# Performance work log

Hardware: AMD Instinct MI355X
Metric: run time of the kernel (lower is better)

Reference implementation:

```python
import jax, jax.numpy as jnp
import numpy as np

DEPTH, DIM, HEADS, MLP, P, IMG, C = 6, 512, 8, 2048, 16, 224, 3
NPATCH = (IMG // P) ** 2  # 196
EPS = 1e-5


def setup_inputs() -> dict:
    key = jax.random.key(0)
    ks = jax.random.split(key, 16)
    s = 0.02
    return {
        "img": jax.random.normal(ks[0], (64, C, IMG, IMG), jnp.float32),
        "patch_w": jax.random.normal(ks[1], (DIM, C * P * P), jnp.float32) * s,
        "patch_b": jax.random.normal(ks[2], (DIM,), jnp.float32) * s,
        "cls_token": jax.random.normal(ks[3], (1, 1, DIM), jnp.float32),
        "pos_emb": jax.random.normal(ks[4], (1, NPATCH + 1, DIM), jnp.float32),
        "in_proj_w": jax.random.normal(ks[5], (DEPTH, 3 * DIM, DIM), jnp.float32) * s,
        "in_proj_b": jax.random.normal(ks[6], (DEPTH, 3 * DIM), jnp.float32) * s,
        "out_proj_w": jax.random.normal(ks[7], (DEPTH, DIM, DIM), jnp.float32) * s,
        "out_proj_b": jax.random.normal(ks[8], (DEPTH, DIM), jnp.float32) * s,
        "ln1_w": jnp.ones((DEPTH, DIM), jnp.float32),
        "ln1_b": jnp.zeros((DEPTH, DIM), jnp.float32),
        "fc1_w": jax.random.normal(ks[9], (DEPTH, MLP, DIM), jnp.float32) * s,
        "fc1_b": jax.random.normal(ks[10], (DEPTH, MLP), jnp.float32) * s,
        "fc2_w": jax.random.normal(ks[11], (DEPTH, DIM, MLP), jnp.float32) * s,
        "fc2_b": jax.random.normal(ks[12], (DEPTH, DIM), jnp.float32) * s,
        "ln2_w": jnp.ones((DEPTH, DIM), jnp.float32),
        "ln2_b": jnp.zeros((DEPTH, DIM), jnp.float32),
    }


def _ln(x, w, b):
    m = jnp.mean(x, -1, keepdims=True)
    v = jnp.mean(jnp.square(x - m), -1, keepdims=True)
    return (x - m) * jax.lax.rsqrt(v + EPS) * w + b


def _patchify(img):
    # b c (h p1) (w p2) -> b (h w) (p1 p2 c), lucidrains ViT ordering
    B = img.shape[0]
    g = IMG // P
    x = img.reshape(B, C, g, P, g, P)
    x = x.transpose(0, 2, 4, 3, 5, 1)  # B, h, w, p1, p2, c
    return x.reshape(B, g * g, P * P * C)


def _vit(img, patch_w, patch_b, cls_token, pos_emb, in_proj_w, in_proj_b,
         out_proj_w, out_proj_b, ln1_w, ln1_b, fc1_w, fc1_b, fc2_w, fc2_b,
         ln2_w, ln2_b):
    B = img.shape[0]
    hd = DIM // HEADS
    x = _patchify(img) @ patch_w.T + patch_b          # [B, 196, 512]
    cls = jnp.broadcast_to(cls_token, (B, 1, DIM))
    x = jnp.concatenate([cls, x], axis=1) + pos_emb   # [B, 197, 512]
    N = x.shape[1]
    for i in range(DEPTH):
        res = x
        qkv = x @ in_proj_w[i].T + in_proj_b[i]       # [B, N, 3*512]
        q, k, v = jnp.split(qkv, 3, axis=-1)
        q = q.reshape(B, N, HEADS, hd).transpose(0, 2, 1, 3)
        k = k.reshape(B, N, HEADS, hd).transpose(0, 2, 1, 3)
        v = v.reshape(B, N, HEADS, hd).transpose(0, 2, 1, 3)
        scores = jnp.einsum('bhnd,bhmd->bhnm', q, k) / jnp.sqrt(jnp.float32(hd))
        probs = jax.nn.softmax(scores, axis=-1)
        ctx = jnp.einsum('bhnm,bhmd->bhnd', probs, v)
        ctx = ctx.transpose(0, 2, 1, 3).reshape(B, N, DIM)
        x = ctx @ out_proj_w[i].T + out_proj_b[i] + res
        x = _ln(x, ln1_w[i], ln1_b[i])
        res = x
        h = jax.nn.gelu(x @ fc1_w[i].T + fc1_b[i], approximate=False)
        x = h @ fc2_w[i].T + fc2_b[i] + res
        x = _ln(x, ln2_w[i], ln2_b[i])
    return x[:, 0]  # ToCLS_Slice: forward returns CLS token [B, 512]


def reference(img, patch_w, patch_b, cls_token, pos_emb, in_proj_w, in_proj_b,
              out_proj_w, out_proj_b, ln1_w, ln1_b, fc1_w, fc1_b, fc2_w, fc2_b,
              ln2_w, ln2_b):
    return _vit(img, patch_w, patch_b, cls_token, pos_emb, in_proj_w, in_proj_b,
                out_proj_w, out_proj_b, ln1_w, ln1_b, fc1_w, fc1_b, fc2_w, fc2_b,
                ln2_w, ln2_b)
```

## Files before the change

kernel.cpp:

```cpp
#include <hip/hip_runtime.h>
#include <hip/hip_bf16.h>

typedef __hip_bfloat16 hb;
typedef __bf16 bf16x8 __attribute__((ext_vector_type(8)));
typedef float f32x4 __attribute__((ext_vector_type(4)));

#define N_DEPTH 6
#define N_DIM   512
#define N_HEADS 8
#define N_MLP   2048
#define N_TOK   197
#define N_PATCH 196
#define N_BATCH 64
#define ROWS    (N_BATCH * N_TOK)
#define ROWS_PAD 12672
#define PROWS   (N_BATCH * N_PATCH)

#define OFF_WPATCH 0u
#define OFF_WQKV   786432u
#define OFF_WOUT   10223616u
#define OFF_WFC1   13369344u
#define OFF_WFC2   25952256u
#define OFF_XBF    38535168u
#define OFF_CTX    51511296u
#define OFF_BIG    64487424u
#define OFF_XF     116391936u
#define OFF_H1     142344192u

__device__ __forceinline__ void gl2lds(const hb* g, hb* l) {
    __builtin_amdgcn_global_load_lds((const __attribute__((address_space(1))) unsigned int*)g,
                                     (__attribute__((address_space(3))) unsigned int*)l, 16, 0, 0);
}


__global__ void cvt_bf16_kernel(const float* __restrict__ in, hb* __restrict__ out, int n) {
    int t = blockIdx.x * 256 + threadIdx.x;
    if (t < n) out[t] = __float2bfloat16(in[t]);
}

__global__ void patchify_kernel(const float* __restrict__ img, hb* __restrict__ Xp) {
    int t = blockIdx.x * 256 + threadIdx.x;
    if (t >= PROWS * 768) return;
    int r = t / 768, j = t % 768;
    int b = r / 196, p = r % 196;
    int ph = p / 14, pw = p % 14;
    int p1 = j / 48, jr = j % 48;
    int p2 = jr / 3, c = jr % 3;
    float v = img[(((size_t)b * 3 + c) * 224 + ph * 16 + p1) * 224 + pw * 16 + p2];
    Xp[t] = __float2bfloat16(v);
}

__global__ void cls_init_kernel(const float* __restrict__ cls, const float* __restrict__ pos,
                                float* __restrict__ xf, hb* __restrict__ xb) {
    int t = blockIdx.x * 256 + threadIdx.x;
    int b = t >> 9, c = t & 511;
    float v = cls[c] + pos[c];
    size_t off = ((size_t)b * N_TOK) * N_DIM + c;
    xf[off] = v;
    xb[off] = __float2bfloat16(v);
}

__global__ void zero_pads_kernel(float* __restrict__ xf, hb* __restrict__ xb, hb* __restrict__ ctx) {
    int t = blockIdx.x * 256 + threadIdx.x;
    size_t off = (size_t)ROWS * N_DIM + t;
    xf[off] = 0.f;
    xb[off] = __float2bfloat16(0.f);
    ctx[off] = __float2bfloat16(0.f);
}

__global__ void extract_cls_kernel(const float* __restrict__ xf, float* __restrict__ out) {
    int t = blockIdx.x * 256 + threadIdx.x;
    int b = t >> 9, c = t & 511;
    out[t] = xf[((size_t)b * N_TOK) * N_DIM + c];
}


__global__ void __launch_bounds__(256) ln_kernel(const float* __restrict__ in,
                                                 const float* __restrict__ w, const float* __restrict__ b,
                                                 float* __restrict__ outf, hb* __restrict__ outb, int rows) {
    int row = blockIdx.x * 4 + (threadIdx.x >> 6);
    int lane = threadIdx.x & 63;
    if (row >= rows) return;
    const float* p = in + (size_t)row * N_DIM;
    float4 v0 = *(const float4*)(p + lane * 8);
    float4 v1 = *(const float4*)(p + lane * 8 + 4);
    float xs[8] = {v0.x, v0.y, v0.z, v0.w, v1.x, v1.y, v1.z, v1.w};
    float s = 0.f, q = 0.f;
#pragma unroll
    for (int j = 0; j < 8; ++j) { s += xs[j]; q += xs[j] * xs[j]; }
#pragma unroll
    for (int o = 32; o > 0; o >>= 1) { s += __shfl_xor(s, o); q += __shfl_xor(q, o); }
    float mean = s * (1.f / 512.f);
    float var = q * (1.f / 512.f) - mean * mean;
    float r = rsqrtf(var + 1e-5f);
    float4 w0 = *(const float4*)(w + lane * 8);
    float4 w1 = *(const float4*)(w + lane * 8 + 4);
    float4 b0 = *(const float4*)(b + lane * 8);
    float4 b1 = *(const float4*)(b + lane * 8 + 4);
    float ws8[8] = {w0.x, w0.y, w0.z, w0.w, w1.x, w1.y, w1.z, w1.w};
    float bs8[8] = {b0.x, b0.y, b0.z, b0.w, b1.x, b1.y, b1.z, b1.w};
    float of[8] __attribute__((aligned(16)));
    hb tb[8] __attribute__((aligned(16)));
#pragma unroll
    for (int j = 0; j < 8; ++j) {
        float y = (xs[j] - mean) * r * ws8[j] + bs8[j];
        of[j] = y;
        tb[j] = __float2bfloat16(y);
    }
    *(float4*)(outf + (size_t)row * N_DIM + lane * 8)     = *(const float4*)&of[0];
    *(float4*)(outf + (size_t)row * N_DIM + lane * 8 + 4) = *(const float4*)&of[4];
    *(float4*)(outb + (size_t)row * N_DIM + lane * 8)     = *(const float4*)&tb[0];
}


template <int MODE>
__global__ void __launch_bounds__(256) gemm_bt(const hb* __restrict__ A, const hb* __restrict__ B,
                                               const float* __restrict__ bias, int K, int N,
                                               hb* __restrict__ outb, float* __restrict__ outf,
                                               const float* __restrict__ res, const float* __restrict__ pos,
                                               hb* __restrict__ vtg) {
    __shared__ hb Sm[8192];
    hb* As = Sm;
    hb* Bs = Sm + 4096;
    const int tid = threadIdx.x;
    const int lane = tid & 63, wid = tid >> 6;
    const int wr = wid >> 1, wc = wid & 1;
    const int quad = lane >> 4, r16 = lane & 15;
    const int m0 = blockIdx.y * 128, n0 = blockIdx.x * 128;

    const int r0 = lane >> 2, c0 = lane & 3;
    const hb* ga0 = A + (size_t)(m0 + wid * 32 + r0) * K + c0 * 8;
    const hb* ga1 = ga0 + (size_t)16 * K;
    const hb* gb0 = B + (size_t)(n0 + wid * 32 + r0) * K + c0 * 8;
    const hb* gb1 = gb0 + (size_t)16 * K;
    hb* la0 = As + (wid * 32) * 32;
    hb* la1 = As + (wid * 32 + 16) * 32;
    hb* lb0 = Bs + (wid * 32) * 32;
    hb* lb1 = Bs + (wid * 32 + 16) * 32;

    f32x4 acc[4][4] = {};

    for (int k0 = 0; k0 < K; k0 += 32) {
        gl2lds(ga0, la0);
        gl2lds(ga1, la1);
        gl2lds(gb0, lb0);
        gl2lds(gb1, lb1);
        ga0 += 32; ga1 += 32; gb0 += 32; gb1 += 32;
        __syncthreads();
        bf16x8 af[4], bfr[4];
#pragma unroll
        for (int t = 0; t < 4; ++t) {
            af[t]  = *(const bf16x8*)&As[(wr * 64 + t * 16 + r16) * 32 + quad * 8];
            bfr[t] = *(const bf16x8*)&Bs[(wc * 64 + t * 16 + r16) * 32 + quad * 8];
        }
#pragma unroll
        for (int mi = 0; mi < 4; ++mi)
#pragma unroll
            for (int nj = 0; nj < 4; ++nj)
                acc[mi][nj] = __builtin_amdgcn_mfma_f32_16x16x32_bf16(af[mi], bfr[nj], acc[mi][nj], 0, 0, 0);
        __syncthreads();
    }

    if constexpr (MODE == 0 || MODE == 1) {
        const bool isv = (MODE == 0) && (n0 >= 1024);
        if (!isv) {
            hb* Cb = Sm + wid * 2048;
#pragma unroll
            for (int p = 0; p < 2; ++p) {
#pragma unroll
                for (int nj2 = 0; nj2 < 2; ++nj2) {
                    int nj = p * 2 + nj2;
                    float bv = bias[n0 + wc * 64 + nj * 16 + r16];
#pragma unroll
                    for (int mi = 0; mi < 4; ++mi)
#pragma unroll
                        for (int e = 0; e < 4; ++e) {
                            float v = acc[mi][nj][e] + bv;
                            if constexpr (MODE == 1)
                                v = 0.5f * v * (1.f + erff(v * 0.70710678118654752f));
                            Cb[(mi * 16 + quad * 4 + e) * 32 + nj2 * 16 + r16] = __float2bfloat16(v);
                        }
                }
#pragma unroll
                for (int it = 0; it < 4; ++it) {
                    int idx = it * 64 + lane;
                    int row = idx >> 2, ch = idx & 3;
                    bf16x8 val = *(const bf16x8*)&Cb[row * 32 + ch * 8];
                    *(bf16x8*)(outb + (size_t)(m0 + wr * 64 + row) * N + n0 + wc * 64 + p * 32 + ch * 8) = val;
                }
            }
        } else {
#pragma unroll
            for (int mi = 0; mi < 4; ++mi) {
#pragma unroll
                for (int e = 0; e < 4; ++e) {
                    int row = m0 + wr * 64 + mi * 16 + quad * 4 + e;
                    int bb = row / 197;
                    int mm = row - bb * 197;
#pragma unroll
                    for (int nj = 0; nj < 4; ++nj) {
                        int col = n0 + wc * 64 + nj * 16 + r16;
                        float v = acc[mi][nj][e] + bias[col];
                        hb hv = __float2bfloat16(v);
                        outb[(size_t)row * N + col] = hv;
                        if (bb < 64) {
                            int d = col - 1024;
                            vtg[((size_t)(bb * 8 + (d >> 6))) * (64 * 224) + (size_t)(d & 63) * 224 + mm] = hv;
                        }
                    }
                }
            }
        }
    } else {
#pragma unroll
        for (int nj = 0; nj < 4; ++nj) {
            int col = n0 + wc * 64 + nj * 16 + r16;
            float bv = bias[col];
#pragma unroll
            for (int mi = 0; mi < 4; ++mi) {
#pragma unroll
                for (int e = 0; e < 4; ++e) {
                    int row = m0 + wr * 64 + mi * 16 + quad * 4 + e;
                    float v = acc[mi][nj][e] + bv;
                    if constexpr (MODE == 2) {
                        v += res[(size_t)row * N + col];
                        outf[(size_t)row * N + col] = v;
                    } else {
                        int pidx = row % 196;
                        int row2 = row + row / 196 + 1;
                        v += pos[(size_t)(pidx + 1) * N_DIM + col];
                        outf[(size_t)row2 * N_DIM + col] = v;
                        outb[(size_t)row2 * N_DIM + col] = __float2bfloat16(v);
                    }
                }
            }
        }
    }
}


__global__ void __launch_bounds__(256, 2) attn_kernel(const hb* __restrict__ qkv,
                                                      const hb* __restrict__ vtg,
                                                      hb* __restrict__ ctx) {
    __shared__ hb Ks[224 * 64];
    __shared__ hb Vt[64 * 224];
    __shared__ hb Pb[4][16 * 40];
    const int bh = blockIdx.x;
    const int b = bh >> 3, h = bh & 7;
    const int tid = threadIdx.x, lane = tid & 63, wid = tid >> 6;
    const int quad = lane >> 4, r16 = lane & 15;
    const hb* base = qkv + (size_t)(b * N_TOK) * 1536 + h * 64;
    const hb* vbase = vtg + (size_t)bh * (64 * 224);

#pragma unroll
    for (int i = 0; i < 7; ++i) {
        int idx = tid + i * 256;
        int m = idx >> 3, c = idx & 7;
        bf16x8 val = {};
        if (m < 197) val = *(const bf16x8*)(base + (size_t)m * 1536 + 512 + c * 8);
        *(bf16x8*)&Ks[m * 64 + c * 8] = val;
    }
#pragma unroll
    for (int i = 0; i < 6; ++i) {
        int idx = tid + i * 256;
        int d = idx / 24, mc = idx % 24;
        *(bf16x8*)&Vt[d * 224 + mc * 8] = *(const bf16x8*)(vbase + d * 224 + mc * 8);
    }
    const hb hzero = __float2bfloat16(0.f);
#pragma unroll
    for (int i = 0; i < 8; ++i) {
        int idx = tid + i * 256;
        int d = idx >> 5, m = 192 + (idx & 31);
        Vt[d * 224 + m] = (m < 197) ? vbase[d * 224 + m] : hzero;
    }

    bf16x8 af[4][2];
#pragma unroll
    for (int mi = 0; mi < 4; ++mi) {
        int q = wid * 64 + mi * 16 + r16;
#pragma unroll
        for (int kc = 0; kc < 2; ++kc)
            af[mi][kc] = *(const bf16x8*)(base + (size_t)q * 1536 + kc * 32 + quad * 8);
    }

    f32x4 o[4][4] = {};
    float mst[4][4], lp[4][4];
#pragma unroll
    for (int mi = 0; mi < 4; ++mi)
#pragma unroll
        for (int e = 0; e < 4; ++e) { mst[mi][e] = -3.0e38f; lp[mi][e] = 0.f; }

    __syncthreads();

    for (int kt = 0; kt < 7; ++kt) {
        bf16x8 bk[2][2], bv[4];
#pragma unroll
        for (int nj = 0; nj < 2; ++nj)
#pragma unroll
            for (int kc = 0; kc < 2; ++kc)
                bk[nj][kc] = *(const bf16x8*)&Ks[(kt * 32 + nj * 16 + r16) * 64 + kc * 32 + quad * 8];
#pragma unroll
        for (int jd = 0; jd < 4; ++jd)
            bv[jd] = *(const bf16x8*)&Vt[(jd * 16 + r16) * 224 + kt * 32 + quad * 8];

        const bool v0 = (kt * 32 + r16) < N_TOK;
        const bool v1 = (kt * 32 + 16 + r16) < N_TOK;

#pragma unroll
        for (int mi = 0; mi < 4; ++mi) {
            f32x4 z = {};
            f32x4 s0v = __builtin_amdgcn_mfma_f32_16x16x32_bf16(af[mi][0], bk[0][0], z, 0, 0, 0);
            s0v = __builtin_amdgcn_mfma_f32_16x16x32_bf16(af[mi][1], bk[0][1], s0v, 0, 0, 0);
            f32x4 s1v = __builtin_amdgcn_mfma_f32_16x16x32_bf16(af[mi][0], bk[1][0], z, 0, 0, 0);
            s1v = __builtin_amdgcn_mfma_f32_16x16x32_bf16(af[mi][1], bk[1][1], s1v, 0, 0, 0);

            float al[4];
#pragma unroll
            for (int e = 0; e < 4; ++e) {
                float s0 = v0 ? s0v[e] * 0.125f : -1e30f;
                float s1 = v1 ? s1v[e] * 0.125f : -1e30f;
                float mx = fmaxf(s0, s1);
#pragma unroll
                for (int off = 1; off < 16; off <<= 1) mx = fmaxf(mx, __shfl_xor(mx, off));
                float mnew = fmaxf(mst[mi][e], mx);
                float alpha = __expf(mst[mi][e] - mnew);
                mst[mi][e] = mnew;
                float p0 = __expf(s0 - mnew);
                float p1 = __expf(s1 - mnew);
                lp[mi][e] = lp[mi][e] * alpha + p0 + p1;
                al[e] = alpha;
                int prow = (quad * 4 + e) * 40;
                Pb[wid][prow + r16]      = __float2bfloat16(p0);
                Pb[wid][prow + 16 + r16] = __float2bfloat16(p1);
            }
#pragma unroll
            for (int jd = 0; jd < 4; ++jd)
#pragma unroll
                for (int e = 0; e < 4; ++e) o[mi][jd][e] *= al[e];
            bf16x8 ap = *(const bf16x8*)&Pb[wid][r16 * 40 + quad * 8];
#pragma unroll
            for (int jd = 0; jd < 4; ++jd)
                o[mi][jd] = __builtin_amdgcn_mfma_f32_16x16x32_bf16(ap, bv[jd], o[mi][jd], 0, 0, 0);
        }
    }

#pragma unroll
    for (int mi = 0; mi < 4; ++mi) {
        float rl[4];
#pragma unroll
        for (int e = 0; e < 4; ++e) {
            float l = lp[mi][e];
#pragma unroll
            for (int off = 1; off < 16; off <<= 1) l += __shfl_xor(l, off);
            rl[e] = 1.f / l;
        }
        int qrow = wid * 64 + mi * 16 + quad * 4;
#pragma unroll
        for (int e = 0; e < 4; ++e) {
            int q = qrow + e;
            if (q < N_TOK) {
                hb* dst = ctx + ((size_t)(b * N_TOK + q)) * N_DIM + h * 64;
#pragma unroll
                for (int jd = 0; jd < 4; ++jd)
                    dst[jd * 16 + r16] = __float2bfloat16(o[mi][jd][e] * rl[e]);
            }
        }
    }
}


extern "C" void kernel_launch(void* const* d_in, const int* in_sizes, int n_in,
                              void* d_out, int out_size, void* d_ws, size_t ws_size,
                              hipStream_t stream) {
    (void)in_sizes; (void)n_in; (void)out_size; (void)ws_size;
    const float* img     = (const float*)d_in[0];
    const float* patch_w = (const float*)d_in[1];
    const float* patch_b = (const float*)d_in[2];
    const float* cls_t   = (const float*)d_in[3];
    const float* pos     = (const float*)d_in[4];
    const float* w_qkv   = (const float*)d_in[5];
    const float* b_qkv   = (const float*)d_in[6];
    const float* w_out   = (const float*)d_in[7];
    const float* b_out   = (const float*)d_in[8];
    const float* ln1w    = (const float*)d_in[9];
    const float* ln1b    = (const float*)d_in[10];
    const float* w_fc1   = (const float*)d_in[11];
    const float* b_fc1   = (const float*)d_in[12];
    const float* w_fc2   = (const float*)d_in[13];
    const float* b_fc2   = (const float*)d_in[14];
    const float* ln2w    = (const float*)d_in[15];
    const float* ln2b    = (const float*)d_in[16];

    char* ws = (char*)d_ws;
    hb* wPatch = (hb*)(ws + OFF_WPATCH);
    hb* wQKV   = (hb*)(ws + OFF_WQKV);
    hb* wOut   = (hb*)(ws + OFF_WOUT);
    hb* wFc1   = (hb*)(ws + OFF_WFC1);
    hb* wFc2   = (hb*)(ws + OFF_WFC2);
    hb* x_bf   = (hb*)(ws + OFF_XBF);
    hb* ctx    = (hb*)(ws + OFF_CTX);
    hb* Xp     = (hb*)(ws + OFF_BIG);
    hb* qkv    = (hb*)(ws + OFF_BIG);
    hb* hmid   = (hb*)(ws + OFF_BIG);
    float* x_f = (float*)(ws + OFF_XF);
    float* h1  = (float*)(ws + OFF_H1);
    hb* vtg    = (hb*)(ws + OFF_H1);

    auto cvt = [&](const float* src, hb* dst, int n) {
        cvt_bf16_kernel<<<dim3((n + 255) / 256), dim3(256), 0, stream>>>(src, dst, n);
    };
    cvt(patch_w, wPatch, 512 * 768);
    cvt(w_qkv, wQKV, N_DEPTH * 1536 * 512);
    cvt(w_out, wOut, N_DEPTH * 512 * 512);
    cvt(w_fc1, wFc1, N_DEPTH * 2048 * 512);
    cvt(w_fc2, wFc2, N_DEPTH * 512 * 2048);

    patchify_kernel<<<dim3((PROWS * 768 + 255) / 256), dim3(256), 0, stream>>>(img, Xp);
    gemm_bt<3><<<dim3(4, 98), dim3(256), 0, stream>>>(Xp, wPatch, patch_b, 768, 512, x_bf, x_f, nullptr, pos, nullptr);
    cls_init_kernel<<<dim3(128), dim3(256), 0, stream>>>(cls_t, pos, x_f, x_bf);
    zero_pads_kernel<<<dim3(128), dim3(256), 0, stream>>>(x_f, x_bf, ctx);

    for (int i = 0; i < N_DEPTH; ++i) {
        gemm_bt<0><<<dim3(12, 99), dim3(256), 0, stream>>>(x_bf, wQKV + (size_t)i * 1536 * 512,
                                                           b_qkv + i * 1536, 512, 1536, qkv, nullptr, nullptr, nullptr, vtg);
        attn_kernel<<<dim3(512), dim3(256), 0, stream>>>(qkv, vtg, ctx);
        gemm_bt<2><<<dim3(4, 99), dim3(256), 0, stream>>>(ctx, wOut + (size_t)i * 512 * 512,
                                                          b_out + i * 512, 512, 512, nullptr, h1, x_f, nullptr, nullptr);
        ln_kernel<<<dim3(3152), dim3(256), 0, stream>>>(h1, ln1w + i * 512, ln1b + i * 512, x_f, x_bf, ROWS);
        gemm_bt<1><<<dim3(16, 99), dim3(256), 0, stream>>>(x_bf, wFc1 + (size_t)i * 2048 * 512,
                                                           b_fc1 + i * 2048, 512, 2048, hmid, nullptr, nullptr, nullptr, nullptr);
        gemm_bt<2><<<dim3(4, 99), dim3(256), 0, stream>>>(hmid, wFc2 + (size_t)i * 512 * 2048,
                                                          b_fc2 + i * 512, 2048, 512, nullptr, h1, x_f, nullptr, nullptr);
        ln_kernel<<<dim3(3152), dim3(256), 0, stream>>>(h1, ln2w + i * 512, ln2b + i * 512, x_f, x_bf, ROWS);
    }

    extract_cls_kernel<<<dim3(128), dim3(256), 0, stream>>>(x_f, (float*)d_out);
}
```

Measured before the change: 1.746 ms.

## Split-K the out-proj and FC2 GEMMs, fuse partial sum into LayerNorm, tanh GELU

```diff
diff --git a/kernel.cpp b/kernel.cpp
--- a/kernel.cpp
+++ b/kernel.cpp
@@ -26,6 +26,8 @@
 #define OFF_BIG    64487424u
 #define OFF_XF     116391936u
 #define OFF_H1     142344192u
+#define OFF_EXTRA  168296448u
+#define WS_NEED_SPLIT (OFF_EXTRA + 25952256u)
 
 __device__ __forceinline__ void gl2lds(const hb* g, hb* l) {
     __builtin_amdgcn_global_load_lds((const __attribute__((address_space(1))) unsigned int*)g,
@@ -75,7 +77,9 @@
 }
 
 
+template <int SUM>
 __global__ void __launch_bounds__(256) ln_kernel(const float* __restrict__ in,
+                                                 const float* __restrict__ in2,
                                                  const float* __restrict__ w, const float* __restrict__ b,
                                                  float* __restrict__ outf, hb* __restrict__ outb, int rows) {
     int row = blockIdx.x * 4 + (threadIdx.x >> 6);
@@ -85,6 +89,13 @@
     float4 v0 = *(const float4*)(p + lane * 8);
     float4 v1 = *(const float4*)(p + lane * 8 + 4);
     float xs[8] = {v0.x, v0.y, v0.z, v0.w, v1.x, v1.y, v1.z, v1.w};
+    if constexpr (SUM) {
+        const float* p2 = in2 + (size_t)row * N_DIM;
+        float4 u0 = *(const float4*)(p2 + lane * 8);
+        float4 u1 = *(const float4*)(p2 + lane * 8 + 4);
+        xs[0] += u0.x; xs[1] += u0.y; xs[2] += u0.z; xs[3] += u0.w;
+        xs[4] += u1.x; xs[5] += u1.y; xs[6] += u1.z; xs[7] += u1.w;
+    }
     float s = 0.f, q = 0.f;
 #pragma unroll
     for (int j = 0; j < 8; ++j) { s += xs[j]; q += xs[j] * xs[j]; }
@@ -115,8 +126,9 @@
 
 template <int MODE>
 __global__ void __launch_bounds__(256) gemm_bt(const hb* __restrict__ A, const hb* __restrict__ B,
-                                               const float* __restrict__ bias, int K, int N,
+                                               const float* __restrict__ bias, int Kstride, int halfK, int N,
                                                hb* __restrict__ outb, float* __restrict__ outf,
+                                               float* __restrict__ outf2,
                                                const float* __restrict__ res, const float* __restrict__ pos,
                                                hb* __restrict__ vtg) {
     __shared__ hb Sm[8192];
@@ -127,12 +139,13 @@
     const int wr = wid >> 1, wc = wid & 1;
     const int quad = lane >> 4, r16 = lane & 15;
     const int m0 = blockIdx.y * 128, n0 = blockIdx.x * 128;
+    const int kb = blockIdx.z * halfK;
 
     const int r0 = lane >> 2, c0 = lane & 3;
-    const hb* ga0 = A + (size_t)(m0 + wid * 32 + r0) * K + c0 * 8;
-    const hb* ga1 = ga0 + (size_t)16 * K;
-    const hb* gb0 = B + (size_t)(n0 + wid * 32 + r0) * K + c0 * 8;
-    const hb* gb1 = gb0 + (size_t)16 * K;
+    const hb* ga0 = A + (size_t)(m0 + wid * 32 + r0) * Kstride + kb + c0 * 8;
+    const hb* ga1 = ga0 + (size_t)16 * Kstride;
+    const hb* gb0 = B + (size_t)(n0 + wid * 32 + r0) * Kstride + kb + c0 * 8;
+    const hb* gb1 = gb0 + (size_t)16 * Kstride;
     hb* la0 = As + (wid * 32) * 32;
     hb* la1 = As + (wid * 32 + 16) * 32;
     hb* lb0 = Bs + (wid * 32) * 32;
@@ -140,7 +153,7 @@
 
     f32x4 acc[4][4] = {};
 
-    for (int k0 = 0; k0 < K; k0 += 32) {
+    for (int k0 = 0; k0 < halfK; k0 += 32) {
         gl2lds(ga0, la0);
         gl2lds(ga1, la1);
         gl2lds(gb0, lb0);
@@ -176,8 +189,11 @@
 #pragma unroll
                         for (int e = 0; e < 4; ++e) {
                             float v = acc[mi][nj][e] + bv;
-                            if constexpr (MODE == 1)
-                                v = 0.5f * v * (1.f + erff(v * 0.70710678118654752f));
+                            if constexpr (MODE == 1) {
+                                float y = 0.79788456f * (v + 0.044715f * v * v * v);
+                                float t = 1.f - 2.f / (__expf(2.f * y) + 1.f);
+                                v = 0.5f * v * (1.f + t);
+                            }
                             Cb[(mi * 16 + quad * 4 + e) * 32 + nj2 * 16 + r16] = __float2bfloat16(v);
                         }
                 }
@@ -211,29 +227,50 @@
                 }
             }
         }
+    } else if constexpr (MODE == 2) {
+        if (blockIdx.z == 0) {
+#pragma unroll
+            for (int nj = 0; nj < 4; ++nj) {
+                int col = n0 + wc * 64 + nj * 16 + r16;
+                float bv = bias[col];
+#pragma unroll
+                for (int mi = 0; mi < 4; ++mi)
+#pragma unroll
+                    for (int e = 0; e < 4; ++e) {
+                        int row = m0 + wr * 64 + mi * 16 + quad * 4 + e;
+                        outf[(size_t)row * N + col] = acc[mi][nj][e] + bv + res[(size_t)row * N + col];
+                    }
+            }
+        } else {
+#pragma unroll
+            for (int nj = 0; nj < 4; ++nj) {
+                int col = n0 + wc * 64 + nj * 16 + r16;
+#pragma unroll
+                for (int mi = 0; mi < 4; ++mi)
+#pragma unroll
+                    for (int e = 0; e < 4; ++e) {
+                        int row = m0 + wr * 64 + mi * 16 + quad * 4 + e;
+                        outf2[(size_t)row * N + col] = acc[mi][nj][e];
+                    }
+            }
+        }
     } else {
 #pragma unroll
         for (int nj = 0; nj < 4; ++nj) {
             int col = n0 + wc * 64 + nj * 16 + r16;
             float bv = bias[col];
 #pragma unroll
-            for (int mi = 0; mi < 4; ++mi) {
+            for (int mi = 0; mi < 4; ++mi)
 #pragma unroll
                 for (int e = 0; e < 4; ++e) {
                     int row = m0 + wr * 64 + mi * 16 + quad * 4 + e;
                     float v = acc[mi][nj][e] + bv;
-                    if constexpr (MODE == 2) {
-                        v += res[(size_t)row * N + col];
-                        outf[(size_t)row * N + col] = v;
-                    } else {
-                        int pidx = row % 196;
-                        int row2 = row + row / 196 + 1;
-                        v += pos[(size_t)(pidx + 1) * N_DIM + col];
-                        outf[(size_t)row2 * N_DIM + col] = v;
-                        outb[(size_t)row2 * N_DIM + col] = __float2bfloat16(v);
-                    }
+                    int pidx = row % 196;
+                    int row2 = row + row / 196 + 1;
+                    v += pos[(size_t)(pidx + 1) * N_DIM + col];
+                    outf[(size_t)row2 * N_DIM + col] = v;
+                    outb[(size_t)row2 * N_DIM + col] = __float2bfloat16(v);
                 }
-            }
         }
     }
 }
@@ -372,7 +409,7 @@
 extern "C" void kernel_launch(void* const* d_in, const int* in_sizes, int n_in,
                               void* d_out, int out_size, void* d_ws, size_t ws_size,
                               hipStream_t stream) {
-    (void)in_sizes; (void)n_in; (void)out_size; (void)ws_size;
+    (void)in_sizes; (void)n_in; (void)out_size;
     const float* img     = (const float*)d_in[0];
     const float* patch_w = (const float*)d_in[1];
     const float* patch_b = (const float*)d_in[2];
@@ -402,9 +439,12 @@
     hb* Xp     = (hb*)(ws + OFF_BIG);
     hb* qkv    = (hb*)(ws + OFF_BIG);
     hb* hmid   = (hb*)(ws + OFF_BIG);
+    float* bigf = (float*)(ws + OFF_BIG);
     float* x_f = (float*)(ws + OFF_XF);
     float* h1  = (float*)(ws + OFF_H1);
     hb* vtg    = (hb*)(ws + OFF_H1);
+    float* extraf = (float*)(ws + OFF_EXTRA);
+    const bool fc2_split = (ws_size >= WS_NEED_SPLIT);
 
     auto cvt = [&](const float* src, hb* dst, int n) {
         cvt_bf16_kernel<<<dim3((n + 255) / 256), dim3(256), 0, stream>>>(src, dst, n);
@@ -416,22 +456,34 @@
     cvt(w_fc2, wFc2, N_DEPTH * 512 * 2048);
 
     patchify_kernel<<<dim3((PROWS * 768 + 255) / 256), dim3(256), 0, stream>>>(img, Xp);
-    gemm_bt<3><<<dim3(4, 98), dim3(256), 0, stream>>>(Xp, wPatch, patch_b, 768, 512, x_bf, x_f, nullptr, pos, nullptr);
+    gemm_bt<3><<<dim3(4, 98), dim3(256), 0, stream>>>(Xp, wPatch, patch_b, 768, 768, 512,
+                                                      x_bf, x_f, nullptr, nullptr, pos, nullptr);
     cls_init_kernel<<<dim3(128), dim3(256), 0, stream>>>(cls_t, pos, x_f, x_bf);
     zero_pads_kernel<<<dim3(128), dim3(256), 0, stream>>>(x_f, x_bf, ctx);
 
     for (int i = 0; i < N_DEPTH; ++i) {
         gemm_bt<0><<<dim3(12, 99), dim3(256), 0, stream>>>(x_bf, wQKV + (size_t)i * 1536 * 512,
-                                                           b_qkv + i * 1536, 512, 1536, qkv, nullptr, nullptr, nullptr, vtg);
+                                                           b_qkv + i * 1536, 512, 512, 1536,
+                                                           qkv, nullptr, nullptr, nullptr, nullptr, vtg);
         attn_kernel<<<dim3(512), dim3(256), 0, stream>>>(qkv, vtg, ctx);
-        gemm_bt<2><<<dim3(4, 99), dim3(256), 0, stream>>>(ctx, wOut + (size_t)i * 512 * 512,
-                                                          b_out + i * 512, 512, 512, nullptr, h1, x_f, nullptr, nullptr);
-        ln_kernel<<<dim3(3152), dim3(256), 0, stream>>>(h1, ln1w + i * 512, ln1b + i * 512, x_f, x_bf, ROWS);
+        gemm_bt<2><<<dim3(4, 99, 2), dim3(256), 0, stream>>>(ctx, wOut + (size_t)i * 512 * 512,
+                                                             b_out + i * 512, 512, 256, 512,
+                                                             nullptr, h1, bigf, x_f, nullptr, nullptr);
+        ln_kernel<1><<<dim3(3152), dim3(256), 0, stream>>>(h1, bigf, ln1w + i * 512, ln1b + i * 512, x_f, x_bf, ROWS);
         gemm_bt<1><<<dim3(16, 99), dim3(256), 0, stream>>>(x_bf, wFc1 + (size_t)i * 2048 * 512,
-                                                           b_fc1 + i * 2048, 512, 2048, hmid, nullptr, nullptr, nullptr, nullptr);
-        gemm_bt<2><<<dim3(4, 99), dim3(256), 0, stream>>>(hmid, wFc2 + (size_t)i * 512 * 2048,
-                                                          b_fc2 + i * 512, 2048, 512, nullptr, h1, x_f, nullptr, nullptr);
-        ln_kernel<<<dim3(3152), dim3(256), 0, stream>>>(h1, ln2w + i * 512, ln2b + i * 512, x_f, x_bf, ROWS);
+                                                           b_fc1 + i * 2048, 512, 512, 2048,
+                                                           hmid, nullptr, nullptr, nullptr, nullptr, nullptr);
+        if (fc2_split) {
+            gemm_bt<2><<<dim3(4, 99, 2), dim3(256), 0, stream>>>(hmid, wFc2 + (size_t)i * 512 * 2048,
+                                                                 b_fc2 + i * 512, 2048, 1024, 512,
+                                                                 nullptr, h1, extraf, x_f, nullptr, nullptr);
+            ln_kernel<1><<<dim3(3152), dim3(256), 0, stream>>>(h1, extraf, ln2w + i * 512, ln2b + i * 512, x_f, x_bf, ROWS);
+        } else {
+            gemm_bt<2><<<dim3(4, 99, 1), dim3(256), 0, stream>>>(hmid, wFc2 + (size_t)i * 512 * 2048,
+                                                                 b_fc2 + i * 512, 2048, 2048, 512,
+                                                                 nullptr, h1, nullptr, x_f, nullptr, nullptr);
+            ln_kernel<0><<<dim3(3152), dim3(256), 0, stream>>>(h1, nullptr, ln2w + i * 512, ln2b + i * 512, x_f, x_bf, ROWS);
+        }
     }
 
     extract_cls_kernel<<<dim3(128), dim3(256), 0, stream>>>(x_f, (float*)d_out);
```

Result: slower. 1.832 ms (+4.9%).
